# Kernel optimization log

Hardware: AMD Instinct MI355X
Metric: run time of the kernel (lower is better)

Reference implementation:

```python
import jax, jax.numpy as jnp
import numpy as np

B, T, C = 256, 512, 100   # batch, time steps, classes (blank = C-1)
U = 32                    # max label length


def setup_inputs() -> dict:
    key = jax.random.key(0)
    k1, k2, k3, k4 = jax.random.split(key, 4)
    # softmax probabilities, as produced by the model's final softmax Dense layer
    y_pred = jax.nn.softmax(jax.random.normal(k1, (B, T, C), dtype=jnp.float32), axis=-1)
    labels = jax.random.randint(k2, (B, U), 0, C - 1, dtype=jnp.int32)  # exclude blank
    input_length = jax.random.randint(k3, (B, 1), T - 64, T + 1, dtype=jnp.int32)
    label_length = jax.random.randint(k4, (B, 1), 16, U + 1, dtype=jnp.int32)
    return {"y_pred": y_pred, "labels": labels,
            "input_length": input_length, "label_length": label_length}


def ctc_batch_cost(y_pred, labels, input_length, label_length):
    """Faithful jax port of keras.backend.ctc_batch_cost (blank = num_classes-1).
    Stable log-space forward DP over the extended label sequence."""
    NEG = jnp.float32(-1e30)
    b, t_len, c = y_pred.shape
    u = labels.shape[1]
    s = 2 * u + 1
    blank = c - 1
    # keras applies log(y_pred + epsilon) with epsilon = 1e-7
    logp = jnp.log(y_pred + 1e-7)
    lab = labels.astype(jnp.int32)
    # extended labels: blank, l1, blank, l2, ..., blank  -> [B, S]
    ext = jnp.full((b, s), blank, dtype=jnp.int32).at[:, 1::2].set(lab)
    # per-step emission log-probs for extended labels: [T, B, S]
    emit = jnp.take_along_axis(logp, ext[:, None, :], axis=2)
    emit = jnp.transpose(emit, (1, 0, 2))
    # skip transition s-2 -> s allowed iff ext[s] != blank and ext[s] != ext[s-2]
    prev2 = jnp.concatenate([jnp.full((b, 2), -1, jnp.int32), ext[:, :-2]], axis=1)
    can_skip = (ext != blank) & (ext != prev2)
    llen = label_length.reshape(b).astype(jnp.int32)
    ilen = input_length.reshape(b).astype(jnp.int32)
    valid = jnp.arange(s)[None, :] < (2 * llen[:, None] + 1)  # [B,S]

    alpha = jnp.full((b, s), NEG)
    alpha = alpha.at[:, 0].set(emit[0, :, 0])
    alpha = alpha.at[:, 1].set(jnp.where(llen > 0, emit[0, :, 1], NEG))
    alpha = jnp.where(valid, alpha, NEG)

    def step(alpha, inp):
        t, e = inp  # t: scalar step index, e: [B,S] emissions at step t
        a1 = jnp.concatenate([jnp.full((b, 1), NEG), alpha[:, :-1]], axis=1)
        a2 = jnp.concatenate([jnp.full((b, 2), NEG), alpha[:, :-2]], axis=1)
        a2 = jnp.where(can_skip, a2, NEG)
        new = jnp.logaddexp(jnp.logaddexp(alpha, a1), a2) + e
        new = jnp.where(valid, new, NEG)
        alpha = jnp.where((t < ilen)[:, None], new, alpha)  # freeze past input_length
        return alpha, None

    alpha, _ = jax.lax.scan(step, alpha, (jnp.arange(1, t_len), emit[1:]))

    last = 2 * llen  # index of trailing blank in extended sequence
    a_last = jnp.take_along_axis(alpha, last[:, None], axis=1)[:, 0]
    a_prev = jnp.take_along_axis(alpha, jnp.maximum(last - 1, 0)[:, None], axis=1)[:, 0]
    a_prev = jnp.where(llen > 0, a_prev, NEG)
    ll = jnp.logaddexp(a_last, a_prev)
    return -ll[:, None]  # [B,1], matching ctc_batch_cost


def reference(y_pred, labels, input_length, label_length):
    # CTCLayer.call returns the per-example CTC loss tensor
    return ctc_batch_cost(y_pred, labels, input_length, label_length)
```

## Files before the change

### kernel.cpp

```cpp
#include <hip/hip_runtime.h>


#define B_ 256
#define T_ 512
#define C_ 100
#define U_ 32
#define BLANK_ 99
#define NEG_ (-1e30f)

__device__ __forceinline__ float dpp_shr1(float old_, float src) {
    int r = __builtin_amdgcn_update_dpp(__float_as_int(old_), __float_as_int(src),
                                        0x138, 0xF, 0xF, false);
    return __int_as_float(r);
}
__device__ __forceinline__ float dpp_shl1(float old_, float src) {
    int r = __builtin_amdgcn_update_dpp(__float_as_int(old_), __float_as_int(src),
                                        0x130, 0xF, 0xF, false);
    return __int_as_float(r);
}
__device__ __forceinline__ float bcast_lane(float v, int lane) {
    return __int_as_float(__builtin_amdgcn_readlane(__float_as_int(v), lane));
}

#define ISSUE_F(RV, TB)                                                        \
    _Pragma("unroll")                                                          \
    for (int j = 0; j < 32; ++j) {                                             \
        const float* ga = p + (size_t)((TB) + j) * C_;                         \
        asm volatile("global_load_dword %0, %1, off" : "=v"(RV[j]) : "v"(ga)); \
    }
#define ISSUE_B(RV, TB)                                                        \
    _Pragma("unroll")                                                          \
    for (int j = 0; j < 32; ++j) {                                             \
        const float* ga = p + (size_t)((TB) - j) * C_;                         \
        asm volatile("global_load_dword %0, %1, off" : "=v"(RV[j]) : "v"(ga)); \
    }

#define WAIT_BANK()                                                            \
    asm volatile("s_waitcnt vmcnt(32)" ::: "memory");                          \
    __builtin_amdgcn_sched_barrier(0);

#define FSTEP(RV, T_IDX)                                                       \
    {                                                                          \
        float e   = __builtin_amdgcn_logf((RV) + 1e-7f);                       \
        float eb  = bcast_lane(e, 1);              \
        float up1 = dpp_shr1(a00, a0);                                         \
        float up2 = dpp_shr1(NEG_, up1);                                       \
        up2 = canskip ? up2 : NEG_;                                            \
        float mx  = fmaxf(fmaxf(a0, up1), up2);                                \
        float sum = __builtin_amdgcn_exp2f(a0  - mx)                           \
                  + __builtin_amdgcn_exp2f(up1 - mx)                           \
                  + __builtin_amdgcn_exp2f(up2 - mx);                          \
        float na  = (mx + e) + __builtin_amdgcn_logf(sum);                     \
        const bool upd = ((T_IDX) <= m);                                       \
        a0  = upd ? na         : a0;                                           \
        a00 = upd ? (a00 + eb) : a00;                                          \
    }

#define BSTEP(RV, K)                                                           \
    {                                                                          \
        float e   = __builtin_amdgcn_logf((RV) + 1e-7f);                       \
        float e64 = bcast_lane(e, 0);              \
        float g   = b0 + e;                                                    \
        float g64 = b64 + e64;                                                 \
        float g1  = dpp_shl1(g64, g);                    \
        float g2  = dpp_shl1(NEG_, g1);                  \
        g2 = csb ? g2 : NEG_;                                                  \
        float mx  = fmaxf(fmaxf(g, g1), g2);                                   \
        float sum = __builtin_amdgcn_exp2f(g  - mx)                            \
                  + __builtin_amdgcn_exp2f(g1 - mx)                            \
                  + __builtin_amdgcn_exp2f(g2 - mx);                           \
        float nbv = mx + __builtin_amdgcn_logf(sum);                           \
        const bool upd = ((K) < nb);                                           \
        b0  = upd ? nbv : b0;                                                  \
        b64 = upd ? g64 : b64;                                                 \
    }

__global__ __launch_bounds__(128, 1) void ctc_fwd_kernel(
    const float* __restrict__ y_pred,
    const int*   __restrict__ labels,
    const int*   __restrict__ input_length,
    const int*   __restrict__ label_length,
    float*       __restrict__ out)
{
    const int b    = blockIdx.x;
    const int lane = threadIdx.x & 63;
    const int wid  = threadIdx.x >> 6;

    const int ilen = min(input_length[b], T_);
    const int llen = label_length[b];
    const int m    = (ilen - 1) >> 1;
    const int nb   = ilen - 1 - m;
    const int last = 2 * llen;

    const int* lab = labels + b * U_;

    __shared__ float af[65];
    __shared__ float bf[65];

    float rvA[32], rvB[32];

    if (wid == 0) {
        const int s = lane + 1;
        int  cls;  bool canskip;
        if (s & 1) {
            const int k = s >> 1;
            cls = lab[k];
            const int prev = (k > 0) ? lab[k - 1] : -1;
            canskip = (s >= 3) && (cls != prev);
        } else { cls = BLANK_; canskip = false; }

        const float* p = y_pred + ((size_t)b * T_) * C_ + cls;

        float e0  = __builtin_amdgcn_logf(p[0] + 1e-7f);
        float a0  = (lane == 0) ? e0 : NEG_;
        float a00 = bcast_lane(e0, 1);

        ISSUE_F(rvA, 1)
        #pragma unroll 1
        for (int i = 0; i < 4; ++i) {
            const int tA = 1 + i * 64;
            ISSUE_F(rvB, tA + 32)
            WAIT_BANK()
            #pragma unroll
            for (int j = 0; j < 32; ++j) FSTEP(rvA[j], tA + j)
            ISSUE_F(rvA, tA + 64)
            WAIT_BANK()
            #pragma unroll
            for (int j = 0; j < 32; ++j) FSTEP(rvB[j], tA + 32 + j)
        }
        asm volatile("s_waitcnt vmcnt(0)" ::: "memory");

        af[lane + 1] = a0;
        if (lane == 0) af[0] = a00;
    } else {
        const int st = lane;
        int cls;
        if (st & 1) cls = lab[st >> 1]; else cls = BLANK_;
        bool csb = false;
        if ((st & 1) && st <= 61) {
            const int k2 = (st + 2) >> 1;
            csb = (lab[k2] != lab[k2 - 1]);
        }

        const float* p = y_pred + ((size_t)b * T_) * C_ + cls;

        float b0  = (st == last || st == last - 1) ? 0.0f : NEG_;
        float b64 = (last == 64) ? 0.0f : NEG_;

        const int t0 = ilen - 1;
        ISSUE_B(rvA, t0)
        #pragma unroll 1
        for (int i = 0; i < 4; ++i) {
            const int k0 = i * 64;
            ISSUE_B(rvB, t0 - (k0 + 32))
            WAIT_BANK()
            #pragma unroll
            for (int j = 0; j < 32; ++j) BSTEP(rvA[j], k0 + j)
            ISSUE_B(rvA, t0 - (k0 + 64))
            WAIT_BANK()
            #pragma unroll
            for (int j = 0; j < 32; ++j) BSTEP(rvB[j], k0 + 32 + j)
        }
        asm volatile("s_waitcnt vmcnt(0)" ::: "memory");

        bf[lane] = b0;
        if (lane == 0) bf[64] = b64;
    }

    __syncthreads();

    if (wid == 0) {
        float x   = af[lane] + bf[lane];
        float x64 = af[64] + bf[64];
        float M = x;
        #pragma unroll
        for (int off = 1; off < 64; off <<= 1) M = fmaxf(M, __shfl_xor(M, off));
        M = fmaxf(M, x64);
        float sm = __builtin_amdgcn_exp2f(x - M);
        #pragma unroll
        for (int off = 1; off < 64; off <<= 1) sm += __shfl_xor(sm, off);
        sm += __builtin_amdgcn_exp2f(x64 - M);
        float ll = M + __builtin_amdgcn_logf(sm);
        if (lane == 0) out[b] = -0.69314718055994530942f * ll;
    }
}

extern "C" void kernel_launch(void* const* d_in, const int* in_sizes, int n_in,
                              void* d_out, int out_size, void* d_ws, size_t ws_size,
                              hipStream_t stream) {
    const float* y_pred       = (const float*)d_in[0];
    const int*   labels       = (const int*)d_in[1];
    const int*   input_length = (const int*)d_in[2];
    const int*   label_length = (const int*)d_in[3];
    float*       out          = (float*)d_out;

    hipLaunchKernelGGL(ctc_fwd_kernel, dim3(B_), dim3(128), 0, stream,
                       y_pred, labels, input_length, label_length, out);
}
```

Measured before the change: 27.30 us.

## Fuse two CTC DP time steps into one five-term logsumexp recurrence

Both the forward and backward wavefronts now advance two time steps per iteration. The two-step transition weights are precomputed from the emissions (using sums of raw probabilities under a log for the merged paths), so the serial alpha/beta dependency chain does one logsumexp over five shifted terms per two steps instead of two three-term logsumexps. The goal is to halve the latency-bound serial chain. The cost is more DPP shifts, transcendental ops and per-lane skip predicates, plus a peeled single backward step to handle odd step counts and a changed forward/backward split point.

```diff
diff --git a/kernel.cpp b/kernel.cpp
--- a/kernel.cpp
+++ b/kernel.cpp
@@ -6,7 +6,8 @@
 #define C_ 100
 #define U_ 32
 #define BLANK_ 99
-#define NEG_ (-1e30f)
+#define NEG_  (-1e30f)
+#define NINF_ (-__builtin_inff())
 
 __device__ __forceinline__ float dpp_shr1(float old_, float src) {
     int r = __builtin_amdgcn_update_dpp(__float_as_int(old_), __float_as_int(src),
@@ -34,45 +35,95 @@
         const float* ga = p + (size_t)((TB) - j) * C_;                         \
         asm volatile("global_load_dword %0, %1, off" : "=v"(RV[j]) : "v"(ga)); \
     }
-
 #define WAIT_BANK()                                                            \
     asm volatile("s_waitcnt vmcnt(32)" ::: "memory");                          \
     __builtin_amdgcn_sched_barrier(0);
 
-#define FSTEP(RV, T_IDX)                                                       \
+#define FSTEP2(RV1, RV2, T2)                                                   \
     {                                                                          \
-        float e   = __builtin_amdgcn_logf((RV) + 1e-7f);                       \
-        float eb  = bcast_lane(e, 1);              \
+        float fA  = (RV1) + 1e-7f;                                             \
+        float fB  = (RV2) + 1e-7f;                                             \
+        float e1  = __builtin_amdgcn_logf(fA);                                 \
+        float e2  = __builtin_amdgcn_logf(fB);                                 \
+        float eb1 = bcast_lane(e1, 1);                                         \
+        float eb2 = bcast_lane(e2, 1);                                         \
+        float fb1 = bcast_lane(fA, 1);                                         \
+        float fm1 = dpp_shr1(fb1, fA);                            \
+        float fm2 = dpp_shr1(0.0f, fm1);                          \
+        float m1l = dpp_shr1(eb1, e1);                            \
+        float m2l = dpp_shr1(NEG_, m1l);                          \
+        float W1  = __builtin_amdgcn_logf(fA + fm1);                           \
+        float W2  = cs2 ? __builtin_amdgcn_logf(fm1 + fA + fm2) : m1l;         \
+        float W3  = cs2 ? m2l : (csm1 ? m1l : NINF_);                          \
+        float W4  = cs24 ? m2l : NINF_;                                        \
+        float ee  = eb1 + eb2;                                                 \
         float up1 = dpp_shr1(a00, a0);                                         \
         float up2 = dpp_shr1(NEG_, up1);                                       \
-        up2 = canskip ? up2 : NEG_;                                            \
-        float mx  = fmaxf(fmaxf(a0, up1), up2);                                \
-        float sum = __builtin_amdgcn_exp2f(a0  - mx)                           \
-                  + __builtin_amdgcn_exp2f(up1 - mx)                           \
-                  + __builtin_amdgcn_exp2f(up2 - mx);                          \
-        float na  = (mx + e) + __builtin_amdgcn_logf(sum);                     \
-        const bool upd = ((T_IDX) <= m);                                       \
+        float up3 = dpp_shr1(NEG_, up2);                                       \
+        float up4 = dpp_shr1(NEG_, up3);                                       \
+        float t0  = a0  + e1;                                                  \
+        float t1  = up1 + W1;                                                  \
+        float t2v = up2 + W2;                                                  \
+        float t3  = up3 + W3;                                                  \
+        float t4  = up4 + W4;                                                  \
+        float mx  = fmaxf(fmaxf(fmaxf(t0, t1), fmaxf(t2v, t3)), t4);           \
+        float sum = __builtin_amdgcn_exp2f(t0  - mx)                           \
+                  + __builtin_amdgcn_exp2f(t1  - mx)                           \
+                  + __builtin_amdgcn_exp2f(t2v - mx)                           \
+                  + __builtin_amdgcn_exp2f(t3  - mx)                           \
+                  + __builtin_amdgcn_exp2f(t4  - mx);                          \
+        float na  = mx + __builtin_amdgcn_logf(sum) + e2;                      \
+        const bool upd = ((T2) <= m);                                          \
         a0  = upd ? na         : a0;                                           \
-        a00 = upd ? (a00 + eb) : a00;                                          \
-    }
-
-#define BSTEP(RV, K)                                                           \
+        a00 = upd ? (a00 + ee) : a00;                                          \
+    }
+
+#define BSTEP2(RVA, RVB, Q)                                                    \
     {                                                                          \
-        float e   = __builtin_amdgcn_logf((RV) + 1e-7f);                       \
-        float e64 = bcast_lane(e, 0);              \
-        float g   = b0 + e;                                                    \
-        float g64 = b64 + e64;                                                 \
-        float g1  = dpp_shl1(g64, g);                    \
-        float g2  = dpp_shl1(NEG_, g1);                  \
-        g2 = csb ? g2 : NEG_;                                                  \
-        float mx  = fmaxf(fmaxf(g, g1), g2);                                   \
-        float sum = __builtin_amdgcn_exp2f(g  - mx)                            \
-                  + __builtin_amdgcn_exp2f(g1 - mx)                            \
-                  + __builtin_amdgcn_exp2f(g2 - mx);                           \
-        float nbv = mx + __builtin_amdgcn_logf(sum);                           \
-        const bool upd = ((K) < nb);                                           \
-        b0  = upd ? nbv : b0;                                                  \
-        b64 = upd ? g64 : b64;                                                 \
+        float fA   = (RVA) + 1e-7f;                                            \
+        float fB   = (RVB) + 1e-7f;                                            \
+        float eA   = __builtin_amdgcn_logf(fA);                                \
+        float eB   = __builtin_amdgcn_logf(fB);                                \
+        float eA0  = bcast_lane(eA, 0);                                        \
+        float eB0  = bcast_lane(eB, 0);                                        \
+        float l64  = eA0 + eB0;                                                \
+        float f64B = bcast_lane(fB, 0);                                        \
+        float fBp1 = dpp_shl1(f64B, fB);                          \
+        float fBp2 = dpp_shl1(0.0f, fBp1);                        \
+        float eAp1 = dpp_shl1(eA0, eA);                           \
+        float eAp2 = dpp_shl1(NINF_, eAp1);                                    \
+        float eAp3 = dpp_shl1(NINF_, eAp2);                                    \
+        float eAp4 = dpp_shl1(NINF_, eAp3);                                    \
+        float eBp1 = dpp_shl1(eB0, eB);                                        \
+        float eBp2 = dpp_shl1(NINF_, eBp1);                                    \
+        float S1   = __builtin_amdgcn_logf(fB + fBp1);                         \
+        float S2   = csb ? __builtin_amdgcn_logf(fBp1 + fB + fBp2) : eBp1;     \
+        float S3   = csb ? eBp2 : (csb1 ? eBp1 : NINF_);                       \
+        float S4   = csb24 ? eBp2 : NINF_;                                     \
+        float V0   = eA + eB;                                                  \
+        float V1   = eAp1 + S1;                                                \
+        float V2   = eAp2 + S2;                                                \
+        float V3   = eAp3 + S3;                                                \
+        float V4   = eAp4 + S4;                                                \
+        float d1   = dpp_shl1(b64, b0);                                        \
+        float d2   = dpp_shl1(NEG_, d1);                                       \
+        float d3   = dpp_shl1(NEG_, d2);                                       \
+        float d4   = dpp_shl1(NEG_, d3);                                       \
+        float t0   = b0 + V0;                                                  \
+        float t1   = d1 + V1;                                                  \
+        float t2v  = d2 + V2;                                                  \
+        float t3   = d3 + V3;                                                  \
+        float t4   = d4 + V4;                                                  \
+        float mx   = fmaxf(fmaxf(fmaxf(t0, t1), fmaxf(t2v, t3)), t4);          \
+        float sum  = __builtin_amdgcn_exp2f(t0  - mx)                          \
+                   + __builtin_amdgcn_exp2f(t1  - mx)                          \
+                   + __builtin_amdgcn_exp2f(t2v - mx)                          \
+                   + __builtin_amdgcn_exp2f(t3  - mx)                          \
+                   + __builtin_amdgcn_exp2f(t4  - mx);                         \
+        float nb0  = mx + __builtin_amdgcn_logf(sum);                          \
+        const bool upd = ((Q) < nbh);                                          \
+        b0  = upd ? nb0        : b0;                                           \
+        b64 = upd ? (b64 + l64): b64;                                          \
     }
 
 __global__ __launch_bounds__(128, 1) void ctc_fwd_kernel(
@@ -88,26 +139,29 @@
 
     const int ilen = min(input_length[b], T_);
     const int llen = label_length[b];
-    const int m    = (ilen - 1) >> 1;
+    const int m    = (ilen >> 1) & ~1;
     const int nb   = ilen - 1 - m;
     const int last = 2 * llen;
 
     const int* lab = labels + b * U_;
 
-    __shared__ float af[65];
-    __shared__ float bf[65];
+    __shared__ float af[66];
+    __shared__ float bf[66];
 
     float rvA[32], rvB[32];
 
     if (wid == 0) {
         const int s = lane + 1;
-        int  cls;  bool canskip;
-        if (s & 1) {
-            const int k = s >> 1;
-            cls = lab[k];
-            const int prev = (k > 0) ? lab[k - 1] : -1;
-            canskip = (s >= 3) && (cls != prev);
-        } else { cls = BLANK_; canskip = false; }
+        int cls;
+        if (s & 1) cls = lab[min(s >> 1, U_ - 1)]; else cls = BLANK_;
+        const bool cs2  = (s & 1) && (s >= 3) &&
+                          (lab[min(s >> 1, U_ - 1)] != lab[min((s >> 1) - 1, U_ - 1)]);
+        const int  sm1  = s - 1;
+        const bool csm1 = (sm1 & 1) && (sm1 >= 3) &&
+                          (lab[min(sm1 >> 1, U_ - 1)] != lab[min((sm1 >> 1) - 1, U_ - 1)]);
+        const int  sm2  = s - 2;
+        const bool cs24 = cs2 && (sm2 >= 3) && (sm2 & 1) &&
+                          (lab[min(sm2 >> 1, U_ - 1)] != lab[min((sm2 >> 1) - 1, U_ - 1)]);
 
         const float* p = y_pred + ((size_t)b * T_) * C_ + cls;
 
@@ -122,11 +176,13 @@
             ISSUE_F(rvB, tA + 32)
             WAIT_BANK()
             #pragma unroll
-            for (int j = 0; j < 32; ++j) FSTEP(rvA[j], tA + j)
+            for (int j2 = 0; j2 < 16; ++j2)
+                FSTEP2(rvA[2 * j2], rvA[2 * j2 + 1], tA + 2 * j2 + 1)
             ISSUE_F(rvA, tA + 64)
             WAIT_BANK()
             #pragma unroll
-            for (int j = 0; j < 32; ++j) FSTEP(rvB[j], tA + 32 + j)
+            for (int j2 = 0; j2 < 16; ++j2)
+                FSTEP2(rvB[2 * j2], rvB[2 * j2 + 1], tA + 32 + 2 * j2 + 1)
         }
         asm volatile("s_waitcnt vmcnt(0)" ::: "memory");
 
@@ -135,31 +191,62 @@
     } else {
         const int st = lane;
         int cls;
-        if (st & 1) cls = lab[st >> 1]; else cls = BLANK_;
-        bool csb = false;
-        if ((st & 1) && st <= 61) {
-            const int k2 = (st + 2) >> 1;
-            csb = (lab[k2] != lab[k2 - 1]);
-        }
+        if (st & 1) cls = lab[min(st >> 1, U_ - 1)]; else cls = BLANK_;
+        const bool csb   = (st & 1) && (st <= 61) &&
+                           (lab[min((st + 2) >> 1, U_ - 1)] != lab[min(((st + 2) >> 1) - 1, U_ - 1)]);
+        const int  sp1   = st + 1;
+        const bool csb1  = (sp1 & 1) && (sp1 <= 61) &&
+                           (lab[min((sp1 + 2) >> 1, U_ - 1)] != lab[min(((sp1 + 2) >> 1) - 1, U_ - 1)]);
+        const int  sp2   = st + 2;
+        const bool csb24 = csb && (sp2 & 1) && (sp2 <= 61) &&
+                           (lab[min((sp2 + 2) >> 1, U_ - 1)] != lab[min(((sp2 + 2) >> 1) - 1, U_ - 1)]);
 
         const float* p = y_pred + ((size_t)b * T_) * C_ + cls;
 
         float b0  = (st == last || st == last - 1) ? 0.0f : NEG_;
         float b64 = (last == 64) ? 0.0f : NEG_;
 
-        const int t0 = ilen - 1;
-        ISSUE_B(rvA, t0)
+        const int t0   = ilen - 1;
+        const int dlt  = nb & 1;
+        const int nbh  = nb >> 1;
+        const int t0b  = t0 - dlt;
+
+        if (dlt) {
+            float rpre;
+            {
+                const float* ga = p + (size_t)t0 * C_;
+                asm volatile("global_load_dword %0, %1, off" : "=v"(rpre) : "v"(ga));
+            }
+            asm volatile("s_waitcnt vmcnt(0)" ::: "memory");
+            float e   = __builtin_amdgcn_logf(rpre + 1e-7f);
+            float e64 = bcast_lane(e, 0);
+            float g   = b0 + e;
+            float g64 = b64 + e64;
+            float g1  = dpp_shl1(g64, g);
+            float g2  = dpp_shl1(NEG_, g1);
+            g2 = csb ? g2 : NEG_;
+            float mx  = fmaxf(fmaxf(g, g1), g2);
+            float sum = __builtin_amdgcn_exp2f(g  - mx)
+                      + __builtin_amdgcn_exp2f(g1 - mx)
+                      + __builtin_amdgcn_exp2f(g2 - mx);
+            b0  = mx + __builtin_amdgcn_logf(sum);
+            b64 = g64;
+        }
+
+        ISSUE_B(rvA, t0b)
         #pragma unroll 1
         for (int i = 0; i < 4; ++i) {
             const int k0 = i * 64;
-            ISSUE_B(rvB, t0 - (k0 + 32))
-            WAIT_BANK()
-            #pragma unroll
-            for (int j = 0; j < 32; ++j) BSTEP(rvA[j], k0 + j)
-            ISSUE_B(rvA, t0 - (k0 + 64))
-            WAIT_BANK()
-            #pragma unroll
-            for (int j = 0; j < 32; ++j) BSTEP(rvB[j], k0 + 32 + j)
+            ISSUE_B(rvB, t0b - (k0 + 32))
+            WAIT_BANK()
+            #pragma unroll
+            for (int j2 = 0; j2 < 16; ++j2)
+                BSTEP2(rvA[2 * j2], rvA[2 * j2 + 1], i * 32 + j2)
+            ISSUE_B(rvA, t0b - (k0 + 64))
+            WAIT_BANK()
+            #pragma unroll
+            for (int j2 = 0; j2 < 16; ++j2)
+                BSTEP2(rvB[2 * j2], rvB[2 * j2 + 1], i * 32 + 16 + j2)
         }
         asm volatile("s_waitcnt vmcnt(0)" ::: "memory");
 
```

After: 31.21 us. 1.14x slower.
